# Performance work log

Hardware: AMD Instinct MI355X
Metric: run time of the kernel (lower is better)

The kernel has to match this reference:

```python
import jax, jax.numpy as jnp
import numpy as np


def _fwd_diffs(x, D, scale):
    # forward difference along each of the first D axes, zero at the end, scaled by x.shape[0]
    outs = []
    for d in range(D):
        pad = [(0, 0)] * x.ndim
        pad[d] = (0, 1)
        outs.append(jnp.pad(jnp.diff(x, axis=d), pad) * scale)
    return jnp.stack(outs, 0)


def _bwd_diffs(p, scale):
    # p: [D, *dims, l]; backward difference of p[i] along axis i with the torch narrow/cat semantics
    outs = []
    for i in range(p.shape[0]):
        pi = p[i]
        head = jax.lax.slice_in_dim(pi, 0, pi.shape[i] - 1, axis=i)
        z = jnp.zeros_like(jax.lax.slice_in_dim(pi, 0, 1, axis=i))
        before = jnp.concatenate([head, z], axis=i)
        after = jnp.concatenate([z, head], axis=i)
        outs.append((before - after) * scale)
    return jnp.stack(outs, 0)


def _solver(f, repeats, l, lmbda, nu):
    dims = list(f.shape)
    H = dims[0]
    D = len(dims) - 1
    res = 1.0 / H
    tauu = res / 6.0
    sigmap = res / (3.0 + l)
    sigmas = 1.0
    proj = l * (l - 1) // 2 + l
    tau = 1.0 / (2.0 + proj / 4.0)
    # (k1,k2) interval combinations and the membership matrix M[K,z] = (k1<=z<=k2)
    combos = np.array([(a, b) for a in range(l) for b in range(a, l)], dtype=np.int32)
    k1 = jnp.asarray(combos[:, 0])
    k2 = jnp.asarray(combos[:, 1])
    zz = np.arange(l)
    M = jnp.asarray(((combos[:, :1] <= zz) & (zz <= combos[:, 1:2])).astype(np.float32))  # [proj, l]

    img = jnp.broadcast_to(f[..., None], tuple(dims) + (l,))
    klf = jnp.arange(1, l + 1, dtype=f.dtype) / l - img  # k/l - f
    u = img
    ubar = img
    px = jnp.zeros((D,) + tuple(dims) + (l,), f.dtype)
    pt = jnp.zeros(tuple(dims) + (l,), f.dtype)
    sx = jnp.zeros((D,) + tuple(dims) + (proj,), f.dtype)
    mux = sx
    mubarx = sx
    nrj = jnp.zeros((), f.dtype)
    h_un = u

    for it in range(int(repeats)):
        # ---- parabola: dual ascent on (px,pt) with closed-form cubic (Cardano) projection ----
        musum = jnp.einsum('...p,pz->...z', mux, M)
        ux = px + sigmap * (_fwd_diffs(ubar, D, H) + musum)
        ut = pt + sigmap * (jnp.pad(jnp.diff(ubar, axis=-1), [(0, 0)] * (ubar.ndim - 1) + [(0, 1)]) * l)
        pen = lmbda * klf * klf
        B = 0.25 * jnp.sum(ux * ux, axis=0) - pen
        mask = ut < B
        y = ut + pen
        norm = jnp.sqrt(jnp.sum(ux * ux, axis=0))
        a = 0.5 * norm                                   # 2*0.25*norm
        b = (2.0 / 3.0) * (1.0 - 0.5 * y)
        sb = jnp.sqrt(jnp.maximum(-b, 0.0))              # sqrt(-b), only used where b<0
        d = jnp.where(b < 0, (a - sb ** 3) * (a + sb ** 3), a * a + b ** 3)
        c = jnp.power(a + jnp.sqrt(jnp.maximum(d, 0.0)), 1.0 / 3.0)
        mask1 = (d >= 0) & (c == 0)
        mask3 = d < 0
        sb3 = jnp.where(sb > 0, sb ** 3, 1.0)
        ratio = jnp.clip(a / sb3, -1.0, 1.0)
        c_safe = jnp.where(c == 0, 1.0, c)
        v = jnp.where(mask1, 0.0,
                      jnp.where(mask3, 2.0 * sb * jnp.cos(jnp.arccos(ratio) / 3.0), c - b / c_safe))
        norm_safe = jnp.where(norm == 0, 1.0, norm)
        px = jnp.where(mask[None],
                       jnp.where((norm == 0)[None], 0.0, (2.0 * v / norm_safe)[None] * ux),
                       ux)
        pt = jnp.where(mask, 0.25 * jnp.sum(px * px, axis=0) - pen, ut)

        # ---- l2 projection of s ----
        mx = sx - sigmas * mubarx
        snorm = jnp.sqrt(jnp.sum(mx * mx, axis=0))
        snorm_safe = jnp.where(snorm == 0, 1.0, snorm)
        sx = jnp.where((snorm > nu * H)[None], mx * nu / snorm_safe[None], mx)

        # ---- mu update: per-(k1,k2) partial sums over the label axis via cumsum ----
        cs = jnp.cumsum(px, axis=-1)
        cs = jnp.pad(cs, [(0, 0)] * (px.ndim - 1) + [(1, 0)])
        t = cs[..., k2 + 1] - cs[..., k1]                # [D, *dims, proj]
        mux_new = mux + tau * (sx - t)
        mubarx = 2.0 * mux_new - mux
        mux = mux_new

        # ---- clipping: primal update with box projection and boundary conditions ----
        if it % 10 == 0:
            h_un = u
        dx = _bwd_diffs(px, H)
        head = pt[..., :-1]
        z = jnp.zeros_like(pt[..., :1])
        dt = (jnp.concatenate([head, z], axis=-1) - jnp.concatenate([z, head], axis=-1)) * l
        Dv = u + tauu * (jnp.sum(dx, axis=0) + dt)
        un = jnp.clip(Dv, 0.0, 1.0)
        un = un.at[..., 0].set(1.0).at[..., l - 1].set(0.0)
        ubar = 2.0 * un - u
        u = un
        if it % 10 == 0:
            nrj = jnp.sum(jnp.abs(u - h_un))
    return u, nrj


def setup_inputs() -> dict:
    key = jax.random.key(0)
    H, W = 256, 256
    f = jax.random.uniform(key, (H, W, 1), dtype=jnp.float32)
    return {"f": f, "repeats": 10, "l": 16, "lmbda": 0.5, "nu": 0.1, "tol": 0.0}


def reference(f, repeats, l, lmbda, nu, tol):
    # tol/early-exit: tol=0 so the torch break never fires; iteration count is fixed at `repeats`.
    u, nrj = _solver(f, repeats, l, lmbda, nu)
    denom = float(np.prod(f.shape[:-1])) * l
    return (u, nrj, nrj / denom, 0)
```

## Files before the change

### kernel.cpp

```cpp
#include <hip/hip_runtime.h>

#define HH 256
#define WW 256
#define NPIX (HH*WW)
#define LL 16
#define NL (NPIX*LL)
#define PP 136
#define PP2 (PP*2)
#define NBLK (NPIX/32)

typedef _Float16 half_t;
typedef __attribute__((ext_vector_type(8))) _Float16 half8;

static constexpr float SIGMAP_F = (float)((1.0/256.0)/(3.0+16.0));
static constexpr float TAUU_F   = (float)((1.0/256.0)/6.0);
static constexpr float TAU_F    = (float)(1.0/36.0);

__device__ __forceinline__ float clampf(float x, float lo, float hi){
    return fminf(fmaxf(x, lo), hi);
}
__device__ __forceinline__ half8 h8zero() {
    half8 v;
    #pragma unroll
    for (int i = 0; i < 8; ++i) v[i] = (half_t)0.0f;
    return v;
}

template<int PM>
__device__ __forceinline__ void prox_one(const float* __restrict__ f, int np, int hf,
    const half_t* __restrict__ ubOld, const half_t* __restrict__ pxOld,
    const half_t* __restrict__ ptOld, const half_t* __restrict__ msOld,
    half8& o0, half8& o1, half8& opt)
{
    int z0 = hf << 3;
    int ip = np >> 8, jp = np & (WW-1);
    bool iok = (ip < HH-1), jok = (jp < WW-1);
    size_t base = (size_t)np*LL + z0;
    float fv = f[np];

    float g0c = 0.0f, g1c = 0.0f;
    half8 ubv = h8zero(), ubi = h8zero(), ubj = h8zero();
    float ubz8 = 0.0f;
    half8 ms0v = h8zero(), ms1v = h8zero();
    half8 p0v  = h8zero(), p1v  = h8zero(), ptv = h8zero();
    if (PM == 0) {
        g0c = iok ? (f[np + WW] - fv) * 256.0f : 0.0f;
        g1c = jok ? (f[np + 1]  - fv) * 256.0f : 0.0f;
    } else {
        ubv = *reinterpret_cast<const half8*>(ubOld + base);
        if (iok) ubi = *reinterpret_cast<const half8*>(ubOld + base + (size_t)WW*LL);
        if (jok) ubj = *reinterpret_cast<const half8*>(ubOld + base + LL);
        if (hf == 0) ubz8 = (float)ubOld[base + 8];
        ms0v = *reinterpret_cast<const half8*>(msOld + base);
        ms1v = *reinterpret_cast<const half8*>(msOld + NL + base);
        p0v  = *reinterpret_cast<const half8*>(pxOld + base);
        p1v  = *reinterpret_cast<const half8*>(pxOld + NL + base);
        ptv  = *reinterpret_cast<const half8*>(ptOld + base);
    }

    #pragma unroll
    for (int e = 0; e < 8; ++e) {
        int z = z0 + e;
        float ux0, ux1, ut;
        if (PM == 0) {
            ux0 = SIGMAP_F * g0c;
            ux1 = SIGMAP_F * g1c;
            ut  = 0.0f;
        } else {
            float ub = (float)ubv[e];
            float g0 = iok ? ((float)ubi[e] - ub) * 256.0f : 0.0f;
            float g1 = jok ? ((float)ubj[e] - ub) * 256.0f : 0.0f;
            float ubn = (e < 7) ? (float)ubv[e+1] : ubz8;
            float gt = (z < LL-1) ? (ubn - ub) * 16.0f : 0.0f;
            ux0 = (float)p0v[e] + SIGMAP_F * (g0 + (float)ms0v[e]);
            ux1 = (float)p1v[e] + SIGMAP_F * (g1 + (float)ms1v[e]);
            ut  = (float)ptv[e] + SIGMAP_F * gt;
        }

        float klf = (float)(z + 1) * 0.0625f - fv;
        float pen = 0.5f * klf * klf;

        float n2 = ux0*ux0 + ux1*ux1;
        float B  = 0.25f * n2 - pen;
        bool mask = ut < B;

        float px0 = ux0, px1 = ux1, ptn = ut;
        if (mask) {
            float y    = ut + pen;
            float norm = sqrtf(n2);
            float a    = 0.5f * norm;
            float b    = (2.0f/3.0f) * (1.0f - 0.5f*y);
            float v;
            if (b < 0.0f) {
                float sb  = sqrtf(-b);
                float sb3 = sb*sb*sb;
                float dd  = (a - sb3)*(a + sb3);
                if (dd < 0.0f) {
                    float ratio = clampf(a / sb3, -1.0f, 1.0f);
                    v = 2.0f * sb * cosf(acosf(ratio) * (1.0f/3.0f));
                } else {
                    float c = cbrtf(a + sqrtf(dd));
                    v = (c == 0.0f) ? 0.0f : (c - b/c);
                }
            } else {
                float dd = a*a + b*b*b;
                float c  = cbrtf(a + sqrtf(dd));
                v = (c == 0.0f) ? 0.0f : (c - b/c);
            }
            if (norm == 0.0f) { px0 = 0.0f; px1 = 0.0f; }
            else              { float s = 2.0f*v/norm; px0 = s*ux0; px1 = s*ux1; }
            ptn = 0.25f*(px0*px0 + px1*px1) - pen;
        }
        o0[e]  = (half_t)px0;
        o1[e]  = (half_t)px1;
        opt[e] = (half_t)ptn;
    }
}

#define PH(k)  ((k) < 8 ? (float)ph0[(k)] : (float)ph1[(k)-8])
#define PPV(k) ((k) < 8 ? (float)pp0[(k)] : (float)pp1[(k)-8])

template<int H, int MODE>
__device__ __forceinline__ void do_set(int d, int n, int lane,
    half8 ph0, half8 ph1, half8 pp0, half8 pp1,
    const half_t* __restrict__ muC,
    half_t* __restrict__ muO,
    float* __restrict__ part)
{
    constexpr size_t setbase = (size_t)H * 17 * 2 * NPIX;
    const size_t vb   = setbase + (size_t)n*16 + (size_t)d*8;
    const size_t vb1  = vb + (size_t)16*NPIX;
    const size_t tail = setbase + (size_t)32*NPIX + (size_t)n*2 + (size_t)d;

    half8 mCv0 = h8zero(), mCv1 = h8zero(), mOv0 = h8zero(), mOv1 = h8zero();
    float mCT = 0.0f, mOT = 0.0f;
    if (MODE >= 1) {
        mCv0 = *reinterpret_cast<const half8*>(&muC[vb]);
        mCv1 = *reinterpret_cast<const half8*>(&muC[vb1]);
        mCT  = (float)muC[tail];
    }
    if (MODE == 2) {
        mOv0 = *reinterpret_cast<const half8*>(&muO[vb]);
        mOv1 = *reinterpret_cast<const half8*>(&muO[vb1]);
        mOT  = (float)muO[tail];
    }

    float tsA = 0.0f, tsB = 0.0f, tpA = 0.0f, tpB = 0.0f;
    #pragma unroll
    for (int k = H; k < 16; ++k) tsA += PH(k);
    #pragma unroll
    for (int k = 15-H; k < 16; ++k) tsB += PH(k);
    if (MODE >= 1) {
        #pragma unroll
        for (int k = H; k < 16; ++k) tpA += PPV(k);
        #pragma unroll
        for (int k = 15-H; k < 16; ++k) tpB += PPV(k);
    }

    half8 muo0, muo1;
    half_t muoT = (half_t)0.0f;
    float sA = 0.0f, sB = 0.0f;
    int q = 0;

    #pragma unroll
    for (int z = 15; z >= 0; --z) {
        float m = 0.0f;
        if (z >= H) {
            float mn;
            if (MODE == 0) {
                mn = -TAU_F * tsA;
            } else {
                float mC, mO;
                if (q < 8)       { mC=(float)mCv0[q];   mO=(float)mOv0[q]; }
                else if (q < 16) { mC=(float)mCv1[q-8]; mO=(float)mOv1[q-8]; }
                else             { mC=mCT;              mO=mOT; }
                float sxp = (mC - mO) * 36.0f + tpA;
                float mx  = sxp - (2.0f*mC - mO);
                float mo  = __shfl_xor(mx, 1);
                float snorm = sqrtf(mx*mx + mo*mo);
                if (snorm > 25.6f) mx *= 0.1f / snorm;
                mn = mC + TAU_F*(mx - tsA);
            }
            if (q < 8)       muo0[q]   = (half_t)mn;
            else if (q < 16) muo1[q-8] = (half_t)mn;
            else             muoT      = (half_t)mn;
            sA += mn; m += sA; ++q;
        }
        if (z >= 15-H) {
            float mn;
            if (MODE == 0) {
                mn = -TAU_F * tsB;
            } else {
                float mC, mO;
                if (q < 8)       { mC=(float)mCv0[q];   mO=(float)mOv0[q]; }
                else if (q < 16) { mC=(float)mCv1[q-8]; mO=(float)mOv1[q-8]; }
                else             { mC=mCT;              mO=mOT; }
                float sxp = (mC - mO) * 36.0f + tpB;
                float mx  = sxp - (2.0f*mC - mO);
                float mo  = __shfl_xor(mx, 1);
                float snorm = sqrtf(mx*mx + mo*mo);
                if (snorm > 25.6f) mx *= 0.1f / snorm;
                mn = mC + TAU_F*(mx - tsB);
            }
            if (q < 8)       muo0[q]   = (half_t)mn;
            else if (q < 16) muo1[q-8] = (half_t)mn;
            else             muoT      = (half_t)mn;
            sB += mn; m += sB; ++q;
        }
        if (z >= H+1) {
            tsA -= PH(z);
            if (MODE >= 1) tpA -= PPV(z);
        }
        if (z >= 15-H+1) {
            tsB -= PH(z);
            if (MODE >= 1) tpB -= PPV(z);
        }
        part[H*1024 + z*64 + lane] = m;
    }

    *reinterpret_cast<half8*>(&muO[vb])  = muo0;
    *reinterpret_cast<half8*>(&muO[vb1]) = muo1;
    muO[tail] = muoT;
}

template<int MODE>
__global__ __launch_bounds__(512, 4) void k_iter(
    const float* __restrict__ f,
    const half_t* __restrict__ pxOld, half_t* __restrict__ pxCur,
    const half_t* __restrict__ ptOld, half_t* __restrict__ ptCur,
    const half_t* __restrict__ ubOld, half_t* __restrict__ ubCur,
    const half_t* __restrict__ msOld, half_t* __restrict__ msCur,
    const half_t* __restrict__ muC, half_t* __restrict__ muO,
    float* __restrict__ u, float* __restrict__ out,
    float* __restrict__ nrjPartial)
{
    __shared__ float part[(MODE <= 2) ? 8192 : 1];
    __shared__ __align__(16) half_t lp0[64][24];
    __shared__ __align__(16) half_t lp1[33][24];
    __shared__ __align__(16) half_t lpt[32][24];
    __shared__ float wsum[8];

    int tid = threadIdx.x;
    int b   = blockIdx.x;
    int n0  = b << 5;
    int i0  = n0 >> 8;
    int j0  = n0 & (WW-1);

    if (tid < 130) {
        int pl, np; bool valid = true;
        int hf = tid & 1;
        if (tid < 64)       { pl = tid >> 1;           np = n0 + pl; }
        else if (tid < 128) { pl = 32 + ((tid-64)>>1); np = n0 + (pl-32) - WW; valid = (i0 > 0); }
        else                { pl = 64;                 np = n0 - 1;            valid = (j0 > 0); }
        if (valid) {
            half8 o0, o1, opt;
            prox_one<(MODE==0) ? 0 : 1>(f, np, hf, ubOld, pxOld, ptOld, msOld, o0, o1, opt);
            int z0v = hf << 3;
            if (pl < 64) *reinterpret_cast<half8*>(&lp0[pl][z0v]) = o0;
            if (pl < 32) {
                *reinterpret_cast<half8*>(&lp1[pl][z0v]) = o1;
                *reinterpret_cast<half8*>(&lpt[pl][z0v]) = opt;
                if (MODE <= 2) {
                    *reinterpret_cast<half8*>(pxCur + (size_t)np*LL + z0v)      = o0;
                    *reinterpret_cast<half8*>(pxCur + NL + (size_t)np*LL + z0v) = o1;
                    *reinterpret_cast<half8*>(ptCur + (size_t)np*LL + z0v)      = opt;
                }
            } else if (pl == 64) {
                *reinterpret_cast<half8*>(&lp1[32][z0v]) = o1;
            }
        }
    }

    int wv = tid >> 6, lane = tid & 63, pix = lane >> 1, d = lane & 1;
    int n  = n0 + pix;
    half8 pp0 = h8zero(), pp1 = h8zero();
    if (MODE == 1 || MODE == 2) {
        const half8* ppv = reinterpret_cast<const half8*>(pxOld + (size_t)d*NL + (size_t)n*LL);
        pp0 = ppv[0]; pp1 = ppv[1];
    }
    int t  = b*512 + tid;
    int z  = t & (LL-1);
    int n2 = t >> 4;
    int i2 = n2 >> 8;
    int j2 = n2 & (WW-1);
    float uo = (MODE == 0) ? f[n2] : u[t];

    __syncthreads();

    if (MODE <= 2) {
        const half8* ls = (d == 0) ? reinterpret_cast<const half8*>(&lp0[pix][0])
                                   : reinterpret_cast<const half8*>(&lp1[pix][0]);
        half8 ph0 = ls[0], ph1 = ls[1];

        if      (wv == 0) do_set<0,MODE>(d,n,lane,ph0,ph1,pp0,pp1,muC,muO,part);
        else if (wv == 1) do_set<1,MODE>(d,n,lane,ph0,ph1,pp0,pp1,muC,muO,part);
        else if (wv == 2) do_set<2,MODE>(d,n,lane,ph0,ph1,pp0,pp1,muC,muO,part);
        else if (wv == 3) do_set<3,MODE>(d,n,lane,ph0,ph1,pp0,pp1,muC,muO,part);
        else if (wv == 4) do_set<4,MODE>(d,n,lane,ph0,ph1,pp0,pp1,muC,muO,part);
        else if (wv == 5) do_set<5,MODE>(d,n,lane,ph0,ph1,pp0,pp1,muC,muO,part);
        else if (wv == 6) do_set<6,MODE>(d,n,lane,ph0,ph1,pp0,pp1,muC,muO,part);
        else              do_set<7,MODE>(d,n,lane,ph0,ph1,pp0,pp1,muC,muO,part);

        __syncthreads();

        #pragma unroll
        for (int r = 0; r < 2; ++r) {
            int z2    = (tid >> 6) + r*8;
            int inner = tid & 63;
            float s = 0.0f;
            #pragma unroll
            for (int hh = 0; hh < 8; ++hh) s += part[hh*1024 + z2*64 + inner];
            int d2 = inner & 1, pix2 = inner >> 1;
            msCur[(size_t)d2*NL + ((size_t)n0 + pix2)*LL + z2] = (half_t)s;
        }
    }

    {
        int pl2 = tid >> 4;
        float p0c = (float)lp0[pl2][z];
        float p1c = (float)lp1[pl2][z];
        float p0u = (i2 > 0) ? (float)lp0[32 + pl2][z] : 0.0f;
        float p1l = (j2 > 0) ? ((pl2 > 0) ? (float)lp1[pl2-1][z] : (float)lp1[32][z]) : 0.0f;
        float ptc = (float)lpt[pl2][z];
        float ptm = (z > 0) ? (float)lpt[pl2][z-1] : 0.0f;

        float d0 = ((i2 < HH-1) ? p0c : 0.0f) - p0u;
        float d1 = ((j2 < WW-1) ? p1c : 0.0f) - p1l;
        float dt = ((z < LL-1) ? ptc : 0.0f) - ptm;

        float Dv = uo + TAUU_F * ((d0 + d1) * 256.0f + dt * 16.0f);
        float un = clampf(Dv, 0.0f, 1.0f);
        if (z == 0)     un = 1.0f;
        if (z == LL-1)  un = 0.0f;
        if (MODE == 3) out[t] = un;
        else {
            u[t]     = un;
            ubCur[t] = (half_t)(2.0f*un - uo);
        }

        if (MODE == 0) {
            float v = fabsf(un - uo);
            #pragma unroll
            for (int off = 32; off > 0; off >>= 1) v += __shfl_down(v, off);
            if ((tid & 63) == 0) wsum[wv] = v;
            __syncthreads();
            if (tid == 0) {
                float s = 0.0f;
                #pragma unroll
                for (int q2 = 0; q2 < 8; ++q2) s += wsum[q2];
                nrjPartial[b] = s;
            }
        }
    }
}

__global__ void k_final(const float* __restrict__ nrjPartial, float* __restrict__ out_tail)
{
    float s = 0.0f;
    for (int k = threadIdx.x; k < NBLK; k += 64) s += nrjPartial[k];
    #pragma unroll
    for (int off = 32; off > 0; off >>= 1) s += __shfl_down(s, off);
    if (threadIdx.x == 0) {
        out_tail[0] = s;
        out_tail[1] = s * (1.0f/1048576.0f);
        out_tail[2] = 0.0f;
    }
}

extern "C" void kernel_launch(void* const* d_in, const int* in_sizes, int n_in,
                              void* d_out, int out_size, void* d_ws, size_t ws_size,
                              hipStream_t stream)
{
    const float* f = (const float*)d_in[0];
    float* out = (float*)d_out;

    char* w = (char*)d_ws;
    size_t off = 0;
    auto allocf = [&](size_t nfloats) {
        float* p = (float*)(w + off);
        off += nfloats * sizeof(float);
        return p;
    };
    auto alloch = [&](size_t nhalf) {
        half_t* p = (half_t*)(w + off);
        off += nhalf * sizeof(half_t);
        return p;
    };
    half_t* muA  = alloch((size_t)NPIX * PP2);
    half_t* muB  = alloch((size_t)NPIX * PP2);
    half_t* msA  = alloch(2*(size_t)NL);
    half_t* msB  = alloch(2*(size_t)NL);
    half_t* pxA  = alloch(2*(size_t)NL);
    half_t* pxB  = alloch(2*(size_t)NL);
    half_t* ptA  = alloch((size_t)NL);
    half_t* ptB  = alloch((size_t)NL);
    half_t* ubA  = alloch((size_t)NL);
    half_t* ubB  = alloch((size_t)NL);
    float*  u    = allocf((size_t)NL);
    float*  nrjP = allocf(NBLK);
    (void)ws_size; (void)in_sizes; (void)n_in; (void)out_size;

    half_t *pxO = pxA, *pxC = pxB;
    half_t *ptO = ptA, *ptC = ptB;
    half_t *ubO = ubA, *ubC = ubB;
    half_t *msO = msA, *msC = msB;
    half_t *mC  = muA, *mO  = muB;
    for (int it = 0; it < 10; ++it) {
        if (it == 0)
            k_iter<0><<<NBLK, 512, 0, stream>>>(f, pxO, pxC, ptO, ptC, ubO, ubC,
                                                msO, msC, mC, mO, u, out, nrjP);
        else if (it == 1)
            k_iter<1><<<NBLK, 512, 0, stream>>>(f, pxO, pxC, ptO, ptC, ubO, ubC,
                                                msO, msC, mC, mO, u, out, nrjP);
        else if (it < 9)
            k_iter<2><<<NBLK, 512, 0, stream>>>(f, pxO, pxC, ptO, ptC, ubO, ubC,
                                                msO, msC, mC, mO, u, out, nrjP);
        else
            k_iter<3><<<NBLK, 512, 0, stream>>>(f, pxO, pxC, ptO, ptC, ubO, ubC,
                                                msO, msC, mC, mO, u, out, nrjP);
        { half_t* tmp = pxO; pxO = pxC; pxC = tmp; }
        { half_t* tmp = ptO; ptO = ptC; ptC = tmp; }
        { half_t* tmp = ubO; ubO = ubC; ubC = tmp; }
        { half_t* tmp = msO; msO = msC; msC = tmp; }
        { half_t* tmp = mC;  mC  = mO;  mO  = tmp; }
    }

    k_final<<<1, 64, 0, stream>>>(nrjP, out + NL);
}
```

Before: 406.9 us.

## Spread prox over more threads and prefetch mu loads before barrier

The parabola prox stage now runs on 260 threads with 4 labels each instead of 130 threads with 8, which shortens the serial prox critical path before the barrier. The mu dual loads (muC and muO) are hoisted out of do_set into the kernel prologue and issued before the prox work, so their global-memory latency overlaps the prox computation. The cost is more live registers across the barrier and smaller half4 vector loads in prox, which may lower occupancy under the 512x4 launch bounds.

```diff
diff --git a/kernel.cpp b/kernel.cpp
--- a/kernel.cpp
+++ b/kernel.cpp
@@ -11,6 +11,7 @@
 
 typedef _Float16 half_t;
 typedef __attribute__((ext_vector_type(8))) _Float16 half8;
+typedef __attribute__((ext_vector_type(4))) _Float16 half4;
 
 static constexpr float SIGMAP_F = (float)((1.0/256.0)/(3.0+16.0));
 static constexpr float TAUU_F   = (float)((1.0/256.0)/6.0);
@@ -25,41 +26,46 @@
     for (int i = 0; i < 8; ++i) v[i] = (half_t)0.0f;
     return v;
 }
+__device__ __forceinline__ half4 h4zero() {
+    half4 v;
+    #pragma unroll
+    for (int i = 0; i < 4; ++i) v[i] = (half_t)0.0f;
+    return v;
+}
 
 template<int PM>
-__device__ __forceinline__ void prox_one(const float* __restrict__ f, int np, int hf,
+__device__ __forceinline__ void prox_q4(const float* __restrict__ f, int np, int z0,
     const half_t* __restrict__ ubOld, const half_t* __restrict__ pxOld,
     const half_t* __restrict__ ptOld, const half_t* __restrict__ msOld,
-    half8& o0, half8& o1, half8& opt)
+    half4& o0, half4& o1, half4& opt)
 {
-    int z0 = hf << 3;
     int ip = np >> 8, jp = np & (WW-1);
     bool iok = (ip < HH-1), jok = (jp < WW-1);
     size_t base = (size_t)np*LL + z0;
     float fv = f[np];
 
     float g0c = 0.0f, g1c = 0.0f;
-    half8 ubv = h8zero(), ubi = h8zero(), ubj = h8zero();
-    float ubz8 = 0.0f;
-    half8 ms0v = h8zero(), ms1v = h8zero();
-    half8 p0v  = h8zero(), p1v  = h8zero(), ptv = h8zero();
+    half4 ubv = h4zero(), ubi = h4zero(), ubj = h4zero();
+    float ubn4 = 0.0f;
+    half4 ms0v = h4zero(), ms1v = h4zero();
+    half4 p0v  = h4zero(), p1v  = h4zero(), ptv = h4zero();
     if (PM == 0) {
         g0c = iok ? (f[np + WW] - fv) * 256.0f : 0.0f;
         g1c = jok ? (f[np + 1]  - fv) * 256.0f : 0.0f;
     } else {
-        ubv = *reinterpret_cast<const half8*>(ubOld + base);
-        if (iok) ubi = *reinterpret_cast<const half8*>(ubOld + base + (size_t)WW*LL);
-        if (jok) ubj = *reinterpret_cast<const half8*>(ubOld + base + LL);
-        if (hf == 0) ubz8 = (float)ubOld[base + 8];
-        ms0v = *reinterpret_cast<const half8*>(msOld + base);
-        ms1v = *reinterpret_cast<const half8*>(msOld + NL + base);
-        p0v  = *reinterpret_cast<const half8*>(pxOld + base);
-        p1v  = *reinterpret_cast<const half8*>(pxOld + NL + base);
-        ptv  = *reinterpret_cast<const half8*>(ptOld + base);
-    }
-
-    #pragma unroll
-    for (int e = 0; e < 8; ++e) {
+        ubv = *reinterpret_cast<const half4*>(ubOld + base);
+        if (iok) ubi = *reinterpret_cast<const half4*>(ubOld + base + (size_t)WW*LL);
+        if (jok) ubj = *reinterpret_cast<const half4*>(ubOld + base + LL);
+        if (z0 < 12) ubn4 = (float)ubOld[base + 4];
+        ms0v = *reinterpret_cast<const half4*>(msOld + base);
+        ms1v = *reinterpret_cast<const half4*>(msOld + NL + base);
+        p0v  = *reinterpret_cast<const half4*>(pxOld + base);
+        p1v  = *reinterpret_cast<const half4*>(pxOld + NL + base);
+        ptv  = *reinterpret_cast<const half4*>(ptOld + base);
+    }
+
+    #pragma unroll
+    for (int e = 0; e < 4; ++e) {
         int z = z0 + e;
         float ux0, ux1, ut;
         if (PM == 0) {
@@ -70,7 +76,7 @@
             float ub = (float)ubv[e];
             float g0 = iok ? ((float)ubi[e] - ub) * 256.0f : 0.0f;
             float g1 = jok ? ((float)ubj[e] - ub) * 256.0f : 0.0f;
-            float ubn = (e < 7) ? (float)ubv[e+1] : ubz8;
+            float ubn = (e < 3) ? (float)ubv[e+1] : ubn4;
             float gt = (z < LL-1) ? (ubn - ub) * 16.0f : 0.0f;
             ux0 = (float)p0v[e] + SIGMAP_F * (g0 + (float)ms0v[e]);
             ux1 = (float)p1v[e] + SIGMAP_F * (g1 + (float)ms1v[e]);
@@ -121,30 +127,13 @@
 #define PPV(k) ((k) < 8 ? (float)pp0[(k)] : (float)pp1[(k)-8])
 
 template<int H, int MODE>
-__device__ __forceinline__ void do_set(int d, int n, int lane,
+__device__ __forceinline__ void do_set(int lane,
     half8 ph0, half8 ph1, half8 pp0, half8 pp1,
-    const half_t* __restrict__ muC,
-    half_t* __restrict__ muO,
+    half8 mCv0, half8 mCv1, float mCT,
+    half8 mOv0, half8 mOv1, float mOT,
+    half_t* __restrict__ muO, size_t vb, size_t vb1, size_t tailIx,
     float* __restrict__ part)
 {
-    constexpr size_t setbase = (size_t)H * 17 * 2 * NPIX;
-    const size_t vb   = setbase + (size_t)n*16 + (size_t)d*8;
-    const size_t vb1  = vb + (size_t)16*NPIX;
-    const size_t tail = setbase + (size_t)32*NPIX + (size_t)n*2 + (size_t)d;
-
-    half8 mCv0 = h8zero(), mCv1 = h8zero(), mOv0 = h8zero(), mOv1 = h8zero();
-    float mCT = 0.0f, mOT = 0.0f;
-    if (MODE >= 1) {
-        mCv0 = *reinterpret_cast<const half8*>(&muC[vb]);
-        mCv1 = *reinterpret_cast<const half8*>(&muC[vb1]);
-        mCT  = (float)muC[tail];
-    }
-    if (MODE == 2) {
-        mOv0 = *reinterpret_cast<const half8*>(&muO[vb]);
-        mOv1 = *reinterpret_cast<const half8*>(&muO[vb1]);
-        mOT  = (float)muO[tail];
-    }
-
     float tsA = 0.0f, tsB = 0.0f, tpA = 0.0f, tpB = 0.0f;
     #pragma unroll
     for (int k = H; k < 16; ++k) tsA += PH(k);
@@ -207,20 +196,18 @@
             else             muoT      = (half_t)mn;
             sB += mn; m += sB; ++q;
         }
-        if (z >= H+1) {
-            tsA -= PH(z);
-            if (MODE >= 1) tpA -= PPV(z);
-        }
-        if (z >= 15-H+1) {
-            tsB -= PH(z);
-            if (MODE >= 1) tpB -= PPV(z);
+        if (z >= H+1)    tsA -= PH(z);
+        if (z >= 15-H+1) tsB -= PH(z);
+        if (MODE >= 1) {
+            if (z >= H+1)    tpA -= PPV(z);
+            if (z >= 15-H+1) tpB -= PPV(z);
         }
         part[H*1024 + z*64 + lane] = m;
     }
 
     *reinterpret_cast<half8*>(&muO[vb])  = muo0;
     *reinterpret_cast<half8*>(&muO[vb1]) = muo1;
-    muO[tail] = muoT;
+    muO[tailIx] = muoT;
 }
 
 template<int MODE>
@@ -246,33 +233,25 @@
     int i0  = n0 >> 8;
     int j0  = n0 & (WW-1);
 
-    if (tid < 130) {
-        int pl, np; bool valid = true;
-        int hf = tid & 1;
-        if (tid < 64)       { pl = tid >> 1;           np = n0 + pl; }
-        else if (tid < 128) { pl = 32 + ((tid-64)>>1); np = n0 + (pl-32) - WW; valid = (i0 > 0); }
-        else                { pl = 64;                 np = n0 - 1;            valid = (j0 > 0); }
-        if (valid) {
-            half8 o0, o1, opt;
-            prox_one<(MODE==0) ? 0 : 1>(f, np, hf, ubOld, pxOld, ptOld, msOld, o0, o1, opt);
-            int z0v = hf << 3;
-            if (pl < 64) *reinterpret_cast<half8*>(&lp0[pl][z0v]) = o0;
-            if (pl < 32) {
-                *reinterpret_cast<half8*>(&lp1[pl][z0v]) = o1;
-                *reinterpret_cast<half8*>(&lpt[pl][z0v]) = opt;
-                if (MODE <= 2) {
-                    *reinterpret_cast<half8*>(pxCur + (size_t)np*LL + z0v)      = o0;
-                    *reinterpret_cast<half8*>(pxCur + NL + (size_t)np*LL + z0v) = o1;
-                    *reinterpret_cast<half8*>(ptCur + (size_t)np*LL + z0v)      = opt;
-                }
-            } else if (pl == 64) {
-                *reinterpret_cast<half8*>(&lp1[32][z0v]) = o1;
-            }
-        }
-    }
-
     int wv = tid >> 6, lane = tid & 63, pix = lane >> 1, d = lane & 1;
     int n  = n0 + pix;
+
+    size_t setbase = (size_t)wv * 17 * 2 * NPIX;
+    size_t vb     = setbase + (size_t)n*16 + (size_t)d*8;
+    size_t vb1    = vb + (size_t)16*NPIX;
+    size_t tailIx = setbase + (size_t)32*NPIX + (size_t)n*2 + (size_t)d;
+    half8 mCv0 = h8zero(), mCv1 = h8zero(), mOv0 = h8zero(), mOv1 = h8zero();
+    float mCT = 0.0f, mOT = 0.0f;
+    if (MODE == 1 || MODE == 2) {
+        mCv0 = *reinterpret_cast<const half8*>(&muC[vb]);
+        mCv1 = *reinterpret_cast<const half8*>(&muC[vb1]);
+        mCT  = (float)muC[tailIx];
+    }
+    if (MODE == 2) {
+        mOv0 = *reinterpret_cast<const half8*>(&muO[vb]);
+        mOv1 = *reinterpret_cast<const half8*>(&muO[vb1]);
+        mOT  = (float)muO[tailIx];
+    }
     half8 pp0 = h8zero(), pp1 = h8zero();
     if (MODE == 1 || MODE == 2) {
         const half8* ppv = reinterpret_cast<const half8*>(pxOld + (size_t)d*NL + (size_t)n*LL);
@@ -285,6 +264,30 @@
     int j2 = n2 & (WW-1);
     float uo = (MODE == 0) ? f[n2] : u[t];
 
+    if (tid < 260) {
+        int pl = tid >> 2, qf = tid & 3, z0v = qf << 2;
+        int np; bool valid = true;
+        if (pl < 32)      np = n0 + pl;
+        else if (pl < 64) { np = n0 + (pl-32) - WW; valid = (i0 > 0); }
+        else              { np = n0 - 1;            valid = (j0 > 0); }
+        if (valid) {
+            half4 o0, o1, opt;
+            prox_q4<(MODE==0) ? 0 : 1>(f, np, z0v, ubOld, pxOld, ptOld, msOld, o0, o1, opt);
+            if (pl < 64) *reinterpret_cast<half4*>(&lp0[pl][z0v]) = o0;
+            if (pl < 32) {
+                *reinterpret_cast<half4*>(&lp1[pl][z0v]) = o1;
+                *reinterpret_cast<half4*>(&lpt[pl][z0v]) = opt;
+                if (MODE <= 2) {
+                    *reinterpret_cast<half4*>(pxCur + (size_t)np*LL + z0v)      = o0;
+                    *reinterpret_cast<half4*>(pxCur + NL + (size_t)np*LL + z0v) = o1;
+                    *reinterpret_cast<half4*>(ptCur + (size_t)np*LL + z0v)      = opt;
+                }
+            } else if (pl == 64) {
+                *reinterpret_cast<half4*>(&lp1[32][z0v]) = o1;
+            }
+        }
+    }
+
     __syncthreads();
 
     if (MODE <= 2) {
@@ -292,14 +295,14 @@
                                    : reinterpret_cast<const half8*>(&lp1[pix][0]);
         half8 ph0 = ls[0], ph1 = ls[1];
 
-        if      (wv == 0) do_set<0,MODE>(d,n,lane,ph0,ph1,pp0,pp1,muC,muO,part);
-        else if (wv == 1) do_set<1,MODE>(d,n,lane,ph0,ph1,pp0,pp1,muC,muO,part);
-        else if (wv == 2) do_set<2,MODE>(d,n,lane,ph0,ph1,pp0,pp1,muC,muO,part);
-        else if (wv == 3) do_set<3,MODE>(d,n,lane,ph0,ph1,pp0,pp1,muC,muO,part);
-        else if (wv == 4) do_set<4,MODE>(d,n,lane,ph0,ph1,pp0,pp1,muC,muO,part);
-        else if (wv == 5) do_set<5,MODE>(d,n,lane,ph0,ph1,pp0,pp1,muC,muO,part);
-        else if (wv == 6) do_set<6,MODE>(d,n,lane,ph0,ph1,pp0,pp1,muC,muO,part);
-        else              do_set<7,MODE>(d,n,lane,ph0,ph1,pp0,pp1,muC,muO,part);
+        if      (wv == 0) do_set<0,MODE>(lane,ph0,ph1,pp0,pp1,mCv0,mCv1,mCT,mOv0,mOv1,mOT,muO,vb,vb1,tailIx,part);
+        else if (wv == 1) do_set<1,MODE>(lane,ph0,ph1,pp0,pp1,mCv0,mCv1,mCT,mOv0,mOv1,mOT,muO,vb,vb1,tailIx,part);
+        else if (wv == 2) do_set<2,MODE>(lane,ph0,ph1,pp0,pp1,mCv0,mCv1,mCT,mOv0,mOv1,mOT,muO,vb,vb1,tailIx,part);
+        else if (wv == 3) do_set<3,MODE>(lane,ph0,ph1,pp0,pp1,mCv0,mCv1,mCT,mOv0,mOv1,mOT,muO,vb,vb1,tailIx,part);
+        else if (wv == 4) do_set<4,MODE>(lane,ph0,ph1,pp0,pp1,mCv0,mCv1,mCT,mOv0,mOv1,mOT,muO,vb,vb1,tailIx,part);
+        else if (wv == 5) do_set<5,MODE>(lane,ph0,ph1,pp0,pp1,mCv0,mCv1,mCT,mOv0,mOv1,mOT,muO,vb,vb1,tailIx,part);
+        else if (wv == 6) do_set<6,MODE>(lane,ph0,ph1,pp0,pp1,mCv0,mCv1,mCT,mOv0,mOv1,mOT,muO,vb,vb1,tailIx,part);
+        else              do_set<7,MODE>(lane,ph0,ph1,pp0,pp1,mCv0,mCv1,mCT,mOv0,mOv1,mOT,muO,vb,vb1,tailIx,part);
 
         __syncthreads();
 
```

New measurement: 372.1 us (median of 2 runs). 1.09x faster.
